# Kernel optimization log

Measured on AMD Instinct MI355X. Metric: run time of the kernel, lower is better.

The kernel has to match this reference:

```python
import jax, jax.numpy as jnp
import numpy as np

N_NODES = 50000
N_EDGES = 800000
D_IN = 128
D_OUT = 128
N_GRAPHS = 64
NEG_SLOPE = 0.01  # torch F.leaky_relu default


def gcn_conv(x, W, b, src, dst, n_nodes):
    """PyG GCNConv: linear, add self-loops, symmetric norm, scatter-add, bias."""
    h = x @ W  # [N, D_OUT]
    # degree including self-loop (edge_weight = 1)
    deg = jnp.zeros((n_nodes,), x.dtype).at[dst].add(1.0) + 1.0
    dinv = jax.lax.rsqrt(deg)
    norm = dinv[src] * dinv[dst]           # [E]
    agg = jnp.zeros_like(h).at[dst].add(h[src] * norm[:, None])
    # self-loop contribution: dinv[i]*dinv[i]*h[i] = h[i]/deg[i]
    return agg + h * (1.0 / deg)[:, None] + b


def gcn_branch(x, edge_index, Ws, bs):
    src, dst = edge_index[0], edge_index[1]
    n = x.shape[0]
    for W, b in zip(Ws, bs):
        x = gcn_conv(x, W, b, src, dst, n)
        x = jax.nn.leaky_relu(x, NEG_SLOPE)
        # dropout is identity in eval mode
    return x


def mean_pool(x, batch, num_graphs):
    s = jax.ops.segment_sum(x, batch, num_segments=num_graphs)
    cnt = jax.ops.segment_sum(jnp.ones((x.shape[0],), x.dtype), batch, num_segments=num_graphs)
    return s / jnp.maximum(cnt, 1.0)[:, None]


def setup_inputs() -> dict:
    key = jax.random.key(0)
    ks = jax.random.split(key, 20)
    inp = {
        'x1': jax.random.normal(ks[0], (N_NODES, D_IN), jnp.float32),
        'edge_index1': jax.random.randint(ks[1], (2, N_EDGES), 0, N_NODES, jnp.int64 if jax.config.jax_enable_x64 else jnp.int32),
        'batch1': jnp.sort(jax.random.randint(ks[2], (N_NODES,), 0, N_GRAPHS)),
        'x2': jax.random.normal(ks[3], (N_NODES, D_IN), jnp.float32),
        'edge_index2': jax.random.randint(ks[4], (2, N_EDGES), 0, N_NODES, jnp.int64 if jax.config.jax_enable_x64 else jnp.int32),
        'batch2': jnp.sort(jax.random.randint(ks[5], (N_NODES,), 0, N_GRAPHS)),
    }
    s = 1.0 / np.sqrt(D_IN)
    inp['W1_0'] = jax.random.uniform(ks[6], (D_IN, D_OUT), jnp.float32, -s, s)
    inp['b1_0'] = jnp.zeros((D_OUT,), jnp.float32)
    inp['W1_1'] = jax.random.uniform(ks[7], (D_OUT, D_OUT), jnp.float32, -s, s)
    inp['b1_1'] = jnp.zeros((D_OUT,), jnp.float32)
    inp['W2_0'] = jax.random.uniform(ks[8], (D_IN, D_OUT), jnp.float32, -s, s)
    inp['b2_0'] = jnp.zeros((D_OUT,), jnp.float32)
    inp['W2_1'] = jax.random.uniform(ks[9], (D_OUT, D_OUT), jnp.float32, -s, s)
    inp['b2_1'] = jnp.zeros((D_OUT,), jnp.float32)
    s2 = 1.0 / np.sqrt(2 * D_OUT)
    inp['lin1_W'] = jax.random.uniform(ks[10], (2 * D_OUT, D_OUT), jnp.float32, -s2, s2)
    inp['lin1_b'] = jax.random.uniform(ks[11], (D_OUT,), jnp.float32, -s2, s2)
    s3 = 1.0 / np.sqrt(D_OUT)
    inp['lin2_W'] = jax.random.uniform(ks[12], (D_OUT, 1), jnp.float32, -s3, s3)
    inp['lin2_b'] = jax.random.uniform(ks[13], (1,), jnp.float32, -s3, s3)
    return inp


def reference(x1, edge_index1, batch1, x2, edge_index2, batch2,
              W1_0, b1_0, W1_1, b1_1, W2_0, b2_0, W2_1, b2_1,
              lin1_W, lin1_b, lin2_W, lin2_b):
    h1 = gcn_branch(x1, edge_index1, [W1_0, W1_1], [b1_0, b1_1])
    h1 = mean_pool(h1, batch1, N_GRAPHS)
    h2 = gcn_branch(x2, edge_index2, [W2_0, W2_1], [b2_0, b2_1])
    h2 = mean_pool(h2, batch2, N_GRAPHS)
    h = jnp.concatenate([h1, h2], axis=-1)  # [G, 256]
    h = jax.nn.relu(h @ lin1_W + lin1_b)
    return h @ lin2_W + lin2_b  # [G, 1]
```

## Files before the change

### kernel.cpp

```cpp
#include <hip/hip_runtime.h>
#include <hip/hip_fp16.h>

#define N_NODES 50000
#define N_EDGES 800000
#define D 128
#define N_GRAPHS 64
#define NEG_SLOPE 0.01f
#define ELLW 32
#define OVF_CAP 8192

#define BUCKETS 196
#define NPAD (BUCKETS * 256)
#define EPB 4096
#define BCAP 5120
#define XS 136

typedef _Float16 half8 __attribute__((ext_vector_type(8)));
typedef _Float16 half4 __attribute__((ext_vector_type(4)));
typedef float f32x4 __attribute__((ext_vector_type(4)));
typedef float f32x2 __attribute__((ext_vector_type(2)));

__device__ __forceinline__ int lower_bound_i(const int* __restrict__ arr, int n, int key) {
    int lo = 0, hi = n;
    while (lo < hi) {
        int mid = (lo + hi) >> 1;
        if (arr[mid] < key) lo = mid + 1; else hi = mid;
    }
    return lo;
}

__global__ __launch_bounds__(256) void k_prep(const float* __restrict__ Wa, const float* __restrict__ Wb,
                                              const float* __restrict__ Wc, const float* __restrict__ Wd,
                                              const int* __restrict__ batch1, const int* __restrict__ batch2,
                                              __half* __restrict__ WtH, int* __restrict__ gcnt,
                                              float* __restrict__ pp, int* __restrict__ cntg) {
    const float* Ws[4] = {Wa, Wb, Wc, Wd};
    const float* W = Ws[blockIdx.x];
    __half* o = WtH + (size_t)blockIdx.x * 16384;
    int t = threadIdx.x;
    for (int r = 0; r < 64; r++) {
        int e = r * 256 + t;
        int k = e >> 7, n = e & 127;
        o[n * 128 + k] = __float2half(W[k * 128 + n]);
    }
#pragma unroll
    for (int i = 0; i < 16; i++) pp[blockIdx.x * 4096 + i * 256 + t] = 0.0f;
    if (blockIdx.x == 0) {
        for (int i = t; i < 2 * BUCKETS + 8; i += 256) gcnt[i] = 0;
    }
    if (blockIdx.x == 1) {
        if (t < 64)
            cntg[t] = lower_bound_i(batch1, N_NODES, t + 1) - lower_bound_i(batch1, N_NODES, t);
        else if (t < 128)
            cntg[t] = lower_bound_i(batch2, N_NODES, (t - 64) + 1) - lower_bound_i(batch2, N_NODES, t - 64);
    }
}

__global__ __launch_bounds__(256) void k_part(const int* __restrict__ ei1, const int* __restrict__ ei2,
                                              int* __restrict__ gcnt, int2* __restrict__ bucketed) {
    const int br = blockIdx.y;
    const int* __restrict__ src = (br ? ei2 : ei1);
    const int* __restrict__ dst = src + N_EDGES;
    int* __restrict__ gc = gcnt + br * BUCKETS;
    int2* __restrict__ bk = bucketed + (size_t)br * BUCKETS * BCAP;

    __shared__ int bcnt[BUCKETS];
    __shared__ int bofs[BUCKETS];
    __shared__ int gbase[BUCKETS];
    __shared__ int sc[BUCKETS];
    __shared__ int stot;
    __shared__ int2 stage[EPB];
    const int tid = threadIdx.x;
    const int base = blockIdx.x * EPB;
    for (int b = tid; b < BUCKETS; b += 256) bcnt[b] = 0;
    __syncthreads();
    int d_[16], s_[16], p_[16];
#pragma unroll
    for (int k = 0; k < 16; k++) {
        int i = base + k * 256 + tid;
        bool v = i < N_EDGES;
        d_[k] = v ? dst[i] : -1;
        s_[k] = v ? src[i] : 0;
        p_[k] = 0;
        if (v) p_[k] = atomicAdd(&bcnt[d_[k] >> 8], 1);
    }
    __syncthreads();
    if (tid < BUCKETS) sc[tid] = bcnt[tid];
    __syncthreads();
    for (int off = 1; off < BUCKETS; off <<= 1) {
        int v = (tid < BUCKETS && tid >= off) ? sc[tid - off] : 0;
        __syncthreads();
        if (tid < BUCKETS) sc[tid] += v;
        __syncthreads();
    }
    if (tid < BUCKETS) {
        bofs[tid] = sc[tid] - bcnt[tid];
        gbase[tid] = atomicAdd(&gc[tid], bcnt[tid]);
    }
    if (tid == BUCKETS - 1) stot = sc[tid];
    __syncthreads();
#pragma unroll
    for (int k = 0; k < 16; k++) {
        if (d_[k] >= 0) stage[bofs[d_[k] >> 8] + p_[k]] = make_int2(d_[k], s_[k]);
    }
    __syncthreads();
    int total = stot;
    for (int i = tid; i < total; i += 256) {
        int2 e = stage[i];
        int b = e.x >> 8;
        int dest = gbase[b] + (i - bofs[b]);
        if (dest < BCAP) bk[(size_t)b * BCAP + dest] = e;
    }
}

__global__ __launch_bounds__(256) void k_build(const int* __restrict__ gcnt, const int2* __restrict__ bucketed,
                                               int* __restrict__ cnti, unsigned short* __restrict__ ell,
                                               int2* __restrict__ ovf, int* __restrict__ ocnt) {
    const int br = blockIdx.y;
    const int* __restrict__ gc = gcnt + br * BUCKETS;
    const int2* __restrict__ bk = bucketed + (size_t)br * BUCKETS * BCAP;
    int* __restrict__ ci = cnti + br * NPAD;
    unsigned short* __restrict__ el = ell + (size_t)br * NPAD * ELLW;
    int2* __restrict__ ov = ovf + (size_t)br * OVF_CAP;
    int* __restrict__ oc = ocnt + br;

    __shared__ unsigned short lell[256 * ELLW];
    __shared__ int lcnt[256];
    const int b = blockIdx.x, tid = threadIdx.x;
    lcnt[tid] = 0;
    __syncthreads();
    int nb = min(gc[b], BCAP);
    const int2* __restrict__ bp = bk + (size_t)b * BCAP;
    for (int i = tid; i < nb; i += 256) {
        int2 e = bp[i];
        int dl = e.x & 255;
        int p = atomicAdd(&lcnt[dl], 1);
        if (p < ELLW) {
            lell[dl * ELLW + p] = (unsigned short)e.y;
        } else {
            int o = atomicAdd(oc, 1);
            if (o < OVF_CAP) ov[o] = e;
        }
    }
    __syncthreads();
    ci[b * 256 + tid] = lcnt[tid];
    uint4* eg = (uint4*)(el + (size_t)b * 256 * ELLW);
    const uint4* elc = (const uint4*)lell;
    for (int i = tid; i < 256 * ELLW * 2 / 16; i += 256) eg[i] = elc[i];
}

template <bool FP16IN>
__global__ __launch_bounds__(256) void k_gemm(const void* __restrict__ xin1, const void* __restrict__ xin2,
                                              const __half* __restrict__ WtHall, int layer,
                                              const int* __restrict__ cnti, unsigned char* __restrict__ H8) {
    const int br = blockIdx.y;
    const void* __restrict__ xin = (br ? xin2 : xin1);
    const __half* __restrict__ WtH = WtHall + (size_t)(br * 2 + layer) * 16384;
    const int* __restrict__ cnt = cnti + br * NPAD;
    unsigned char* __restrict__ h = H8 + (size_t)br * N_NODES * 128;

    __shared__ _Float16 Xl[64 * XS];
    __shared__ _Float16 Wt[128 * XS];
    const int tid = threadIdx.x;
    const int w = tid >> 6, lane = tid & 63;
    const int quad = lane >> 4, l16 = lane & 15;
    const int row0 = blockIdx.x * 64;

#pragma unroll
    for (int i = 0; i < 8; i++) {
        int i2 = tid + 256 * i;
        int r = i2 >> 4, cg = i2 & 15;
        *(uint4*)&Wt[r * XS + cg * 8] = ((const uint4*)WtH)[i2];
    }
    if (FP16IN) {
        const __half* x = (const __half*)xin;
#pragma unroll
        for (int i = 0; i < 4; i++) {
            int i2 = tid + 256 * i;
            int r = i2 >> 4, cg = i2 & 15;
            uint4 v = make_uint4(0, 0, 0, 0);
            if (row0 + r < N_NODES) v = ((const uint4*)(x + (size_t)(row0 + r) * D))[cg];
            *(uint4*)&Xl[r * XS + cg * 8] = v;
        }
    } else {
        const float* x = (const float*)xin;
#pragma unroll
        for (int i = 0; i < 8; i++) {
            int i2 = tid + 256 * i;
            int r = i2 >> 5, f4 = i2 & 31;
            float4 v = make_float4(0.f, 0.f, 0.f, 0.f);
            if (row0 + r < N_NODES) v = *(const float4*)((const float*)x + (size_t)(row0 + r) * D + f4 * 4);
            half4 hv;
            hv[0] = (_Float16)v.x; hv[1] = (_Float16)v.y; hv[2] = (_Float16)v.z; hv[3] = (_Float16)v.w;
            *(half4*)&Xl[r * XS + f4 * 4] = hv;
        }
    }
    __syncthreads();

    half8 a[4];
#pragma unroll
    for (int kb = 0; kb < 4; kb++)
        a[kb] = *(const half8*)&Xl[(w * 16 + l16) * XS + kb * 32 + quad * 8];

    const int rbase = row0 + w * 16 + quad * 4;
    float di[4];
#pragma unroll
    for (int reg = 0; reg < 4; reg++) {
        int r = rbase + reg;
        di[reg] = (r < N_NODES) ? rsqrtf((float)cnt[r] + 1.0f) : 0.0f;
    }

    float accs[8][4];
#pragma unroll
    for (int ct = 0; ct < 8; ct++) {
        f32x4 acc = {0.f, 0.f, 0.f, 0.f};
#pragma unroll
        for (int kb = 0; kb < 4; kb++) {
            half8 b = *(const half8*)&Wt[(ct * 16 + l16) * XS + kb * 32 + quad * 8];
            acc = __builtin_amdgcn_mfma_f32_16x16x32_f16(a[kb], b, acc, 0, 0, 0);
        }
#pragma unroll
        for (int reg = 0; reg < 4; reg++) accs[ct][reg] = acc[reg] * di[reg];
    }

    __syncthreads();
    unsigned char* S = (unsigned char*)Xl;
#pragma unroll
    for (int ct = 0; ct < 8; ct++)
#pragma unroll
        for (int reg = 0; reg < 4; reg++) {
            int p = __builtin_amdgcn_cvt_pk_fp8_f32(accs[ct][reg], accs[ct][reg], 0, false);
            S[(w * 16 + quad * 4 + reg) * 128 + ct * 16 + l16] = (unsigned char)p;
        }
    __syncthreads();
#pragma unroll
    for (int i = 0; i < 2; i++) {
        int idx = tid + 256 * i;
        int r = idx >> 3, cg = idx & 7;
        if (row0 + r < N_NODES)
            ((uint4*)(h + (size_t)(row0 + r) * 128))[cg] = ((const uint4*)S)[idx];
    }
}

__global__ __launch_bounds__(256) void k_agg(const int* __restrict__ cnti, const unsigned short* __restrict__ ell,
                                             const int2* __restrict__ ovf, const int* __restrict__ ocnt,
                                             const unsigned char* __restrict__ H8all, const float* __restrict__ bias1,
                                             const float* __restrict__ bias2, __half* __restrict__ ACT) {
    const int br = blockIdx.y;
    const int* __restrict__ cnt = cnti + br * NPAD;
    const unsigned short* __restrict__ el = ell + (size_t)br * NPAD * ELLW;
    const int2* __restrict__ ov = ovf + (size_t)br * OVF_CAP;
    const unsigned char* __restrict__ H8 = H8all + (size_t)br * N_NODES * 128;
    const float* __restrict__ bias = (br ? bias2 : bias1);
    __half* __restrict__ out = ACT + (size_t)br * N_NODES * D;

    const int tid = threadIdx.x;
    const int l32 = tid & 31;
    const int node = blockIdx.x * 8 + (tid >> 5);
    int n = cnt[node];
    int nc = min(n, ELLW);
    int sv = 0;
    if (l32 < nc) sv = (int)el[(size_t)node * ELLW + l32];
    int ncOther = __shfl(nc, (tid & 63) ^ 32, 64);
    int jmax = max(nc, ncOther);

    float4 acc[8];
    {
        unsigned int dw = *(const unsigned int*)(H8 + (size_t)node * 128 + l32 * 4);
        f32x2 lo = __builtin_amdgcn_cvt_pk_f32_fp8((int)dw, false);
        f32x2 hi = __builtin_amdgcn_cvt_pk_f32_fp8((int)dw, true);
        acc[0] = make_float4(lo[0], lo[1], hi[0], hi[1]);
    }
#pragma unroll
    for (int i = 1; i < 8; i++) acc[i] = make_float4(0.f, 0.f, 0.f, 0.f);

    for (int j = 0; j < jmax; j += 8) {
        int s[8]; float w[8];
#pragma unroll
        for (int i = 0; i < 8; i++) {
            s[i] = __shfl(sv, j + i, 32);
            w[i] = ((j + i) < nc) ? 1.0f : 0.0f;
        }
#pragma unroll
        for (int i = 0; i < 8; i++) {
            unsigned int dw = *(const unsigned int*)(H8 + (size_t)s[i] * 128 + l32 * 4);
            f32x2 lo = __builtin_amdgcn_cvt_pk_f32_fp8((int)dw, false);
            f32x2 hi = __builtin_amdgcn_cvt_pk_f32_fp8((int)dw, true);
            acc[i].x = fmaf(w[i], lo[0], acc[i].x);
            acc[i].y = fmaf(w[i], lo[1], acc[i].y);
            acc[i].z = fmaf(w[i], hi[0], acc[i].z);
            acc[i].w = fmaf(w[i], hi[1], acc[i].w);
        }
    }
    if (n > ELLW) {
        int oc = min(ocnt[br], OVF_CAP);
        for (int o = 0; o < oc; o++) {
            int2 p = ov[o];
            if (p.x == node) {
                unsigned int dw = *(const unsigned int*)(H8 + (size_t)p.y * 128 + l32 * 4);
                f32x2 lo = __builtin_amdgcn_cvt_pk_f32_fp8((int)dw, false);
                f32x2 hi = __builtin_amdgcn_cvt_pk_f32_fp8((int)dw, true);
                acc[0].x += lo[0]; acc[0].y += lo[1]; acc[0].z += hi[0]; acc[0].w += hi[1];
            }
        }
    }
    float sx = ((acc[0].x + acc[1].x) + (acc[2].x + acc[3].x)) + ((acc[4].x + acc[5].x) + (acc[6].x + acc[7].x));
    float sy = ((acc[0].y + acc[1].y) + (acc[2].y + acc[3].y)) + ((acc[4].y + acc[5].y) + (acc[6].y + acc[7].y));
    float sz = ((acc[0].z + acc[1].z) + (acc[2].z + acc[3].z)) + ((acc[4].z + acc[5].z) + (acc[6].z + acc[7].z));
    float sw = ((acc[0].w + acc[1].w) + (acc[2].w + acc[3].w)) + ((acc[4].w + acc[5].w) + (acc[6].w + acc[7].w));
    float dv = rsqrtf((float)n + 1.0f);
    float4 b = ((const float4*)bias)[l32];
    float vx = sx * dv + b.x;
    float vy = sy * dv + b.y;
    float vz = sz * dv + b.z;
    float vw = sw * dv + b.w;
    vx = vx > 0.0f ? vx : NEG_SLOPE * vx;
    vy = vy > 0.0f ? vy : NEG_SLOPE * vy;
    vz = vz > 0.0f ? vz : NEG_SLOPE * vz;
    vw = vw > 0.0f ? vw : NEG_SLOPE * vw;
    union { __half2 h2[2]; uint2 u; } up;
    up.h2[0] = __floats2half2_rn(vx, vy);
    up.h2[1] = __floats2half2_rn(vz, vw);
    *(uint2*)(out + (size_t)node * 128 + l32 * 4) = up.u;
}

__global__ __launch_bounds__(256) void k_aggpool(const int* __restrict__ cnti, const unsigned short* __restrict__ ell,
                                                 const int2* __restrict__ ovf, const int* __restrict__ ocnt,
                                                 const unsigned char* __restrict__ H8all,
                                                 const float* __restrict__ bias1, const float* __restrict__ bias2,
                                                 const int* __restrict__ batch1, const int* __restrict__ batch2,
                                                 float* __restrict__ ppall) {
    const int br = blockIdx.y;
    const int* __restrict__ cnt = cnti + br * NPAD;
    const unsigned short* __restrict__ el = ell + (size_t)br * NPAD * ELLW;
    const int2* __restrict__ ov = ovf + (size_t)br * OVF_CAP;
    const unsigned char* __restrict__ H8 = H8all + (size_t)br * N_NODES * 128;
    const float* __restrict__ bias = (br ? bias2 : bias1);
    const int* __restrict__ batch = (br ? batch2 : batch1);
    float* __restrict__ pp = ppall + (size_t)br * N_GRAPHS * D;

    const int tid = threadIdx.x;
    const int l32 = tid & 31;
    const int hw = tid >> 5;
    const int node = blockIdx.x * 8 + hw;
    int n = cnt[node];
    int nc = min(n, ELLW);
    int sv = 0;
    if (l32 < nc) sv = (int)el[(size_t)node * ELLW + l32];
    int ncOther = __shfl(nc, (tid & 63) ^ 32, 64);
    int jmax = max(nc, ncOther);

    float4 acc[8];
    {
        unsigned int dw = *(const unsigned int*)(H8 + (size_t)node * 128 + l32 * 4);
        f32x2 lo = __builtin_amdgcn_cvt_pk_f32_fp8((int)dw, false);
        f32x2 hi = __builtin_amdgcn_cvt_pk_f32_fp8((int)dw, true);
        acc[0] = make_float4(lo[0], lo[1], hi[0], hi[1]);
    }
#pragma unroll
    for (int i = 1; i < 8; i++) acc[i] = make_float4(0.f, 0.f, 0.f, 0.f);

    for (int j = 0; j < jmax; j += 8) {
        int s[8]; float wt[8];
#pragma unroll
        for (int i = 0; i < 8; i++) {
            s[i] = __shfl(sv, j + i, 32);
            wt[i] = ((j + i) < nc) ? 1.0f : 0.0f;
        }
#pragma unroll
        for (int i = 0; i < 8; i++) {
            unsigned int dw = *(const unsigned int*)(H8 + (size_t)s[i] * 128 + l32 * 4);
            f32x2 lo = __builtin_amdgcn_cvt_pk_f32_fp8((int)dw, false);
            f32x2 hi = __builtin_amdgcn_cvt_pk_f32_fp8((int)dw, true);
            acc[i].x = fmaf(wt[i], lo[0], acc[i].x);
            acc[i].y = fmaf(wt[i], lo[1], acc[i].y);
            acc[i].z = fmaf(wt[i], hi[0], acc[i].z);
            acc[i].w = fmaf(wt[i], hi[1], acc[i].w);
        }
    }
    if (n > ELLW) {
        int oc = min(ocnt[br], OVF_CAP);
        for (int o = 0; o < oc; o++) {
            int2 p = ov[o];
            if (p.x == node) {
                unsigned int dw = *(const unsigned int*)(H8 + (size_t)p.y * 128 + l32 * 4);
                f32x2 lo = __builtin_amdgcn_cvt_pk_f32_fp8((int)dw, false);
                f32x2 hi = __builtin_amdgcn_cvt_pk_f32_fp8((int)dw, true);
                acc[0].x += lo[0]; acc[0].y += lo[1]; acc[0].z += hi[0]; acc[0].w += hi[1];
            }
        }
    }
    float sx = ((acc[0].x + acc[1].x) + (acc[2].x + acc[3].x)) + ((acc[4].x + acc[5].x) + (acc[6].x + acc[7].x));
    float sy = ((acc[0].y + acc[1].y) + (acc[2].y + acc[3].y)) + ((acc[4].y + acc[5].y) + (acc[6].y + acc[7].y));
    float sz = ((acc[0].z + acc[1].z) + (acc[2].z + acc[3].z)) + ((acc[4].z + acc[5].z) + (acc[6].z + acc[7].z));
    float sw = ((acc[0].w + acc[1].w) + (acc[2].w + acc[3].w)) + ((acc[4].w + acc[5].w) + (acc[6].w + acc[7].w));
    float dv = rsqrtf((float)n + 1.0f);
    float4 b = ((const float4*)bias)[l32];
    float vx = sx * dv + b.x;
    float vy = sy * dv + b.y;
    float vz = sz * dv + b.z;
    float vw = sw * dv + b.w;
    vx = vx > 0.0f ? vx : NEG_SLOPE * vx;
    vy = vy > 0.0f ? vy : NEG_SLOPE * vy;
    vz = vz > 0.0f ? vz : NEG_SLOPE * vz;
    vw = vw > 0.0f ? vw : NEG_SLOPE * vw;
    __half2 q0 = __floats2half2_rn(vx, vy);
    __half2 q1 = __floats2half2_rn(vz, vw);
    float2 f0 = __half22float2(q0);
    float2 f1 = __half22float2(q1);

    __shared__ float sacc[8][128];
    __shared__ int sg[8];
    *(float4*)&sacc[hw][l32 * 4] = make_float4(f0.x, f0.y, f1.x, f1.y);
    if (l32 == 0) sg[hw] = batch[node];
    __syncthreads();
    if (tid < 128) {
        float s = sacc[0][tid];
        int g = sg[0];
        for (int r2 = 1; r2 < 8; r2++) {
            if (sg[r2] == g) {
                s += sacc[r2][tid];
            } else {
                atomicAdd(&pp[(size_t)g * D + tid], s);
                s = sacc[r2][tid];
                g = sg[r2];
            }
        }
        atomicAdd(&pp[(size_t)g * D + tid], s);
    }
}

__global__ __launch_bounds__(128) void k_mlp(const float* __restrict__ pp, const int* __restrict__ cntg,
                                             const float* __restrict__ lin1W, const float* __restrict__ lin1b,
                                             const float* __restrict__ lin2W, const float* __restrict__ lin2b,
                                             float* __restrict__ out) {
    int g = blockIdx.x;
    int c = threadIdx.x;
    __shared__ float cat[2 * D];
    cat[c] = pp[(size_t)g * D + c] / fmaxf((float)cntg[g], 1.0f);
    cat[c + D] = pp[(size_t)(N_GRAPHS + g) * D + c] / fmaxf((float)cntg[64 + g], 1.0f);
    __syncthreads();
    float acc = lin1b[c];
#pragma unroll 8
    for (int k = 0; k < 2 * D; k++) acc += cat[k] * lin1W[k * D + c];
    acc = fmaxf(acc, 0.0f);
    float v = acc * lin2W[c];
#pragma unroll
    for (int off = 32; off > 0; off >>= 1) v += __shfl_down(v, off, 64);
    __shared__ float wsum[2];
    if ((c & 63) == 0) wsum[c >> 6] = v;
    __syncthreads();
    if (c == 0) out[g] = wsum[0] + wsum[1] + lin2b[0];
}

extern "C" void kernel_launch(void* const* d_in, const int* in_sizes, int n_in,
                              void* d_out, int out_size, void* d_ws, size_t ws_size,
                              hipStream_t stream) {
    const float* x1 = (const float*)d_in[0];
    const int*   ei1 = (const int*)d_in[1];
    const int*   batch1 = (const int*)d_in[2];
    const float* x2 = (const float*)d_in[3];
    const int*   ei2 = (const int*)d_in[4];
    const int*   batch2 = (const int*)d_in[5];
    const float* W1_0 = (const float*)d_in[6];
    const float* b1_0 = (const float*)d_in[7];
    const float* W1_1 = (const float*)d_in[8];
    const float* b1_1 = (const float*)d_in[9];
    const float* W2_0 = (const float*)d_in[10];
    const float* b2_0 = (const float*)d_in[11];
    const float* W2_1 = (const float*)d_in[12];
    const float* b2_1 = (const float*)d_in[13];
    const float* lin1W = (const float*)d_in[14];
    const float* lin1b = (const float*)d_in[15];
    const float* lin2W = (const float*)d_in[16];
    const float* lin2b = (const float*)d_in[17];
    float* out = (float*)d_out;

    __half* WtH = (__half*)d_ws;
    __half* ACT = WtH + 65536;
    unsigned char* H8a = (unsigned char*)(ACT + 2 * (size_t)N_NODES * D);
    unsigned char* H8b = H8a + 2 * (size_t)N_NODES * 128;
    unsigned short* ell = (unsigned short*)(H8b + 2 * (size_t)N_NODES * 128);
    int2*   bucketed = (int2*)(ell + 2 * (size_t)NPAD * ELLW);
    int*    cnti = (int*)(bucketed + 2 * (size_t)BUCKETS * BCAP);
    int*    gcnt = cnti + 2 * NPAD;
    int*    ocnt = gcnt + 2 * BUCKETS;
    int*    cntg = ocnt + 8;
    int2*   ovf  = (int2*)(cntg + 128);
    float*  pp   = (float*)(ovf + 2 * (size_t)OVF_CAP);

    dim3 b256(256);
    int partBlocks = (N_EDGES + EPB - 1) / EPB;
    int gemmBlocks = (N_NODES + 63) / 64;
    int aggBlocks  = N_NODES / 8;

    k_prep<<<4, b256, 0, stream>>>(W1_0, W1_1, W2_0, W2_1, batch1, batch2, WtH, gcnt, pp, cntg);

    k_part  <<<dim3(partBlocks, 2), b256, 0, stream>>>(ei1, ei2, gcnt, bucketed);
    k_build <<<dim3(BUCKETS, 2),    b256, 0, stream>>>(gcnt, bucketed, cnti, ell, ovf, ocnt);

    k_gemm<false><<<dim3(gemmBlocks, 2), b256, 0, stream>>>(x1, x2, WtH, 0, cnti, H8a);
    k_agg        <<<dim3(aggBlocks, 2),  b256, 0, stream>>>(cnti, ell, ovf, ocnt, H8a, b1_0, b2_0, ACT);
    k_gemm<true> <<<dim3(gemmBlocks, 2), b256, 0, stream>>>(ACT, ACT + (size_t)N_NODES * D, WtH, 1, cnti, H8b);
    k_aggpool    <<<dim3(aggBlocks, 2),  b256, 0, stream>>>(cnti, ell, ovf, ocnt, H8b, b1_1, b2_1, batch1, batch2, pp);

    k_mlp<<<N_GRAPHS, dim3(128), 0, stream>>>(pp, cntg, lin1W, lin1b, lin2W, lin2b, out);
}
```

Baseline: 288.6 us.

## Double-buffer neighbor gathers in aggregation, interleave branches, shrink partition blocks

The aggregation kernels now stage each block's neighbor index lists in shared memory and gather neighbor rows with a two-buffer software pipeline over groups of 8. The next group's loads are issued before the current group is accumulated, which is meant to hide gather latency. Branch selection moves from the grid y dimension to interleaving on blockIdx.x. The edge partition kernel processes half as many edges per block to gain more parallelism. The ELL build also zero-fills its shared staging, so unused slots hold index 0 rather than stale data; zero-weight padding slots then read row 0 instead of arbitrary rows. The fixed unroll up to 32 neighbors adds register pressure and code size.

After: 281.2 us, median of 2. 1.03x faster.

```diff
diff --git a/kernel.cpp b/kernel.cpp
--- a/kernel.cpp
+++ b/kernel.cpp
@@ -11,7 +11,7 @@
 
 #define BUCKETS 196
 #define NPAD (BUCKETS * 256)
-#define EPB 4096
+#define EPB 2048
 #define BCAP 5120
 #define XS 136
 
@@ -58,7 +58,8 @@
 
 __global__ __launch_bounds__(256) void k_part(const int* __restrict__ ei1, const int* __restrict__ ei2,
                                               int* __restrict__ gcnt, int2* __restrict__ bucketed) {
-    const int br = blockIdx.y;
+    const int br = blockIdx.x & 1;
+    const int blk = blockIdx.x >> 1;
     const int* __restrict__ src = (br ? ei2 : ei1);
     const int* __restrict__ dst = src + N_EDGES;
     int* __restrict__ gc = gcnt + br * BUCKETS;
@@ -71,12 +72,12 @@
     __shared__ int stot;
     __shared__ int2 stage[EPB];
     const int tid = threadIdx.x;
-    const int base = blockIdx.x * EPB;
+    const int base = blk * EPB;
     for (int b = tid; b < BUCKETS; b += 256) bcnt[b] = 0;
     __syncthreads();
-    int d_[16], s_[16], p_[16];
-#pragma unroll
-    for (int k = 0; k < 16; k++) {
+    int d_[8], s_[8], p_[8];
+#pragma unroll
+    for (int k = 0; k < 8; k++) {
         int i = base + k * 256 + tid;
         bool v = i < N_EDGES;
         d_[k] = v ? dst[i] : -1;
@@ -100,7 +101,7 @@
     if (tid == BUCKETS - 1) stot = sc[tid];
     __syncthreads();
 #pragma unroll
-    for (int k = 0; k < 16; k++) {
+    for (int k = 0; k < 8; k++) {
         if (d_[k] >= 0) stage[bofs[d_[k] >> 8] + p_[k]] = make_int2(d_[k], s_[k]);
     }
     __syncthreads();
@@ -116,7 +117,8 @@
 __global__ __launch_bounds__(256) void k_build(const int* __restrict__ gcnt, const int2* __restrict__ bucketed,
                                                int* __restrict__ cnti, unsigned short* __restrict__ ell,
                                                int2* __restrict__ ovf, int* __restrict__ ocnt) {
-    const int br = blockIdx.y;
+    const int br = blockIdx.x & 1;
+    const int b = blockIdx.x >> 1;
     const int* __restrict__ gc = gcnt + br * BUCKETS;
     const int2* __restrict__ bk = bucketed + (size_t)br * BUCKETS * BCAP;
     int* __restrict__ ci = cnti + br * NPAD;
@@ -126,8 +128,10 @@
 
     __shared__ unsigned short lell[256 * ELLW];
     __shared__ int lcnt[256];
-    const int b = blockIdx.x, tid = threadIdx.x;
+    const int tid = threadIdx.x;
     lcnt[tid] = 0;
+#pragma unroll
+    for (int i = 0; i < 4; i++) ((uint4*)lell)[tid + 256 * i] = make_uint4(0u, 0u, 0u, 0u);
     __syncthreads();
     int nb = min(gc[b], BCAP);
     const int2* __restrict__ bp = bk + (size_t)b * BCAP;
@@ -242,11 +246,67 @@
     }
 }
 
+#define AGG_ISSUE(buf, g) do {                                                             \
+    unsigned int iw0 = *(const unsigned int*)&sidx[hw][(g) * 8 + 0];                       \
+    unsigned int iw1 = *(const unsigned int*)&sidx[hw][(g) * 8 + 2];                       \
+    unsigned int iw2 = *(const unsigned int*)&sidx[hw][(g) * 8 + 4];                       \
+    unsigned int iw3 = *(const unsigned int*)&sidx[hw][(g) * 8 + 6];                       \
+    buf[0] = *(const unsigned int*)(H8 + (size_t)(iw0 & 0xffffu) * 128 + l32 * 4);         \
+    buf[1] = *(const unsigned int*)(H8 + (size_t)(iw0 >> 16) * 128 + l32 * 4);             \
+    buf[2] = *(const unsigned int*)(H8 + (size_t)(iw1 & 0xffffu) * 128 + l32 * 4);         \
+    buf[3] = *(const unsigned int*)(H8 + (size_t)(iw1 >> 16) * 128 + l32 * 4);             \
+    buf[4] = *(const unsigned int*)(H8 + (size_t)(iw2 & 0xffffu) * 128 + l32 * 4);         \
+    buf[5] = *(const unsigned int*)(H8 + (size_t)(iw2 >> 16) * 128 + l32 * 4);             \
+    buf[6] = *(const unsigned int*)(H8 + (size_t)(iw3 & 0xffffu) * 128 + l32 * 4);         \
+    buf[7] = *(const unsigned int*)(H8 + (size_t)(iw3 >> 16) * 128 + l32 * 4);             \
+} while (0)
+
+#define AGG_CONSUME(buf, g) do {                                                           \
+    _Pragma("unroll")                                                                      \
+    for (int i_ = 0; i_ < 8; i_++) {                                                       \
+        float wt = ((g) * 8 + i_ < nc) ? 1.0f : 0.0f;                                      \
+        f32x2 lo = __builtin_amdgcn_cvt_pk_f32_fp8((int)buf[i_], false);                   \
+        f32x2 hi = __builtin_amdgcn_cvt_pk_f32_fp8((int)buf[i_], true);                    \
+        accv[i_ & 3].x = fmaf(wt, lo[0], accv[i_ & 3].x);                                  \
+        accv[i_ & 3].y = fmaf(wt, lo[1], accv[i_ & 3].y);                                  \
+        accv[i_ & 3].z = fmaf(wt, hi[0], accv[i_ & 3].z);                                  \
+        accv[i_ & 3].w = fmaf(wt, hi[1], accv[i_ & 3].w);                                  \
+    }                                                                                      \
+} while (0)
+
+#define AGG_CORE()                                                                         \
+    float4 accv[4];                                                                        \
+    {                                                                                      \
+        f32x2 lo = __builtin_amdgcn_cvt_pk_f32_fp8((int)dself, false);                     \
+        f32x2 hi = __builtin_amdgcn_cvt_pk_f32_fp8((int)dself, true);                      \
+        accv[0] = make_float4(lo[0], lo[1], hi[0], hi[1]);                                 \
+    }                                                                                      \
+    accv[1] = make_float4(0.f, 0.f, 0.f, 0.f); accv[2] = accv[1]; accv[3] = accv[1];       \
+    unsigned int b0_[8], b1_[8];                                                           \
+    AGG_ISSUE(b0_, 0);                                                                     \
+    if (jmax > 8) { AGG_ISSUE(b1_, 1); }                                                   \
+    AGG_CONSUME(b0_, 0);                                                                   \
+    if (jmax > 8) {                                                                        \
+        if (jmax > 16) { AGG_ISSUE(b0_, 2); }                                              \
+        AGG_CONSUME(b1_, 1);                                                               \
+        if (jmax > 16) {                                                                   \
+            if (jmax > 24) { AGG_ISSUE(b1_, 3); }                                          \
+            AGG_CONSUME(b0_, 2);                                                           \
+            if (jmax > 24) { AGG_CONSUME(b1_, 3); }                                        \
+        }                                                                                  \
+    }
+
 __global__ __launch_bounds__(256) void k_agg(const int* __restrict__ cnti, const unsigned short* __restrict__ ell,
                                              const int2* __restrict__ ovf, const int* __restrict__ ocnt,
                                              const unsigned char* __restrict__ H8all, const float* __restrict__ bias1,
                                              const float* __restrict__ bias2, __half* __restrict__ ACT) {
-    const int br = blockIdx.y;
+    const int tid = threadIdx.x;
+    const int l32 = tid & 31;
+    const int hw = tid >> 5;
+    const int br = blockIdx.x & 1;
+    const int blk = blockIdx.x >> 1;
+    const int node = blk * 8 + hw;
+
     const int* __restrict__ cnt = cnti + br * NPAD;
     const unsigned short* __restrict__ el = ell + (size_t)br * NPAD * ELLW;
     const int2* __restrict__ ov = ovf + (size_t)br * OVF_CAP;
@@ -254,44 +314,18 @@
     const float* __restrict__ bias = (br ? bias2 : bias1);
     __half* __restrict__ out = ACT + (size_t)br * N_NODES * D;
 
-    const int tid = threadIdx.x;
-    const int l32 = tid & 31;
-    const int node = blockIdx.x * 8 + (tid >> 5);
+    __shared__ unsigned short sidx[8][ELLW];
+    if (tid < 32) ((uint4*)sidx)[tid] = ((const uint4*)(el + (size_t)blk * 8 * ELLW))[tid];
+
     int n = cnt[node];
     int nc = min(n, ELLW);
-    int sv = 0;
-    if (l32 < nc) sv = (int)el[(size_t)node * ELLW + l32];
-    int ncOther = __shfl(nc, (tid & 63) ^ 32, 64);
-    int jmax = max(nc, ncOther);
-
-    float4 acc[8];
-    {
-        unsigned int dw = *(const unsigned int*)(H8 + (size_t)node * 128 + l32 * 4);
-        f32x2 lo = __builtin_amdgcn_cvt_pk_f32_fp8((int)dw, false);
-        f32x2 hi = __builtin_amdgcn_cvt_pk_f32_fp8((int)dw, true);
-        acc[0] = make_float4(lo[0], lo[1], hi[0], hi[1]);
-    }
-#pragma unroll
-    for (int i = 1; i < 8; i++) acc[i] = make_float4(0.f, 0.f, 0.f, 0.f);
-
-    for (int j = 0; j < jmax; j += 8) {
-        int s[8]; float w[8];
-#pragma unroll
-        for (int i = 0; i < 8; i++) {
-            s[i] = __shfl(sv, j + i, 32);
-            w[i] = ((j + i) < nc) ? 1.0f : 0.0f;
-        }
-#pragma unroll
-        for (int i = 0; i < 8; i++) {
-            unsigned int dw = *(const unsigned int*)(H8 + (size_t)s[i] * 128 + l32 * 4);
-            f32x2 lo = __builtin_amdgcn_cvt_pk_f32_fp8((int)dw, false);
-            f32x2 hi = __builtin_amdgcn_cvt_pk_f32_fp8((int)dw, true);
-            acc[i].x = fmaf(w[i], lo[0], acc[i].x);
-            acc[i].y = fmaf(w[i], lo[1], acc[i].y);
-            acc[i].z = fmaf(w[i], hi[0], acc[i].z);
-            acc[i].w = fmaf(w[i], hi[1], acc[i].w);
-        }
-    }
+    int ncO = __shfl(nc, (tid & 63) ^ 32, 64);
+    int jmax = max(nc, ncO);
+    unsigned int dself = *(const unsigned int*)(H8 + (size_t)node * 128 + l32 * 4);
+    __syncthreads();
+
+    AGG_CORE();
+
     if (n > ELLW) {
         int oc = min(ocnt[br], OVF_CAP);
         for (int o = 0; o < oc; o++) {
@@ -300,14 +334,14 @@
                 unsigned int dw = *(const unsigned int*)(H8 + (size_t)p.y * 128 + l32 * 4);
                 f32x2 lo = __builtin_amdgcn_cvt_pk_f32_fp8((int)dw, false);
                 f32x2 hi = __builtin_amdgcn_cvt_pk_f32_fp8((int)dw, true);
-                acc[0].x += lo[0]; acc[0].y += lo[1]; acc[0].z += hi[0]; acc[0].w += hi[1];
+                accv[0].x += lo[0]; accv[0].y += lo[1]; accv[0].z += hi[0]; accv[0].w += hi[1];
             }
         }
     }
-    float sx = ((acc[0].x + acc[1].x) + (acc[2].x + acc[3].x)) + ((acc[4].x + acc[5].x) + (acc[6].x + acc[7].x));
-    float sy = ((acc[0].y + acc[1].y) + (acc[2].y + acc[3].y)) + ((acc[4].y + acc[5].y) + (acc[6].y + acc[7].y));
-    float sz = ((acc[0].z + acc[1].z) + (acc[2].z + acc[3].z)) + ((acc[4].z + acc[5].z) + (acc[6].z + acc[7].z));
-    float sw = ((acc[0].w + acc[1].w) + (acc[2].w + acc[3].w)) + ((acc[4].w + acc[5].w) + (acc[6].w + acc[7].w));
+    float sx = (accv[0].x + accv[1].x) + (accv[2].x + accv[3].x);
+    float sy = (accv[0].y + accv[1].y) + (accv[2].y + accv[3].y);
+    float sz = (accv[0].z + accv[1].z) + (accv[2].z + accv[3].z);
+    float sw = (accv[0].w + accv[1].w) + (accv[2].w + accv[3].w);
     float dv = rsqrtf((float)n + 1.0f);
     float4 b = ((const float4*)bias)[l32];
     float vx = sx * dv + b.x;
@@ -330,7 +364,13 @@
                                                  const float* __restrict__ bias1, const float* __restrict__ bias2,
                                                  const int* __restrict__ batch1, const int* __restrict__ batch2,
                                                  float* __restrict__ ppall) {
-    const int br = blockIdx.y;
+    const int tid = threadIdx.x;
+    const int l32 = tid & 31;
+    const int hw = tid >> 5;
+    const int br = blockIdx.x & 1;
+    const int blk = blockIdx.x >> 1;
+    const int node = blk * 8 + hw;
+
     const int* __restrict__ cnt = cnti + br * NPAD;
     const unsigned short* __restrict__ el = ell + (size_t)br * NPAD * ELLW;
     const int2* __restrict__ ov = ovf + (size_t)br * OVF_CAP;
@@ -339,45 +379,18 @@
     const int* __restrict__ batch = (br ? batch2 : batch1);
     float* __restrict__ pp = ppall + (size_t)br * N_GRAPHS * D;
 
-    const int tid = threadIdx.x;
-    const int l32 = tid & 31;
-    const int hw = tid >> 5;
-    const int node = blockIdx.x * 8 + hw;
+    __shared__ unsigned short sidx[8][ELLW];
+    if (tid < 32) ((uint4*)sidx)[tid] = ((const uint4*)(el + (size_t)blk * 8 * ELLW))[tid];
+
     int n = cnt[node];
     int nc = min(n, ELLW);
-    int sv = 0;
-    if (l32 < nc) sv = (int)el[(size_t)node * ELLW + l32];
-    int ncOther = __shfl(nc, (tid & 63) ^ 32, 64);
-    int jmax = max(nc, ncOther);
-
-    float4 acc[8];
-    {
-        unsigned int dw = *(const unsigned int*)(H8 + (size_t)node * 128 + l32 * 4);
-        f32x2 lo = __builtin_amdgcn_cvt_pk_f32_fp8((int)dw, false);
-        f32x2 hi = __builtin_amdgcn_cvt_pk_f32_fp8((int)dw, true);
-        acc[0] = make_float4(lo[0], lo[1], hi[0], hi[1]);
-    }
-#pragma unroll
-    for (int i = 1; i < 8; i++) acc[i] = make_float4(0.f, 0.f, 0.f, 0.f);
-
-    for (int j = 0; j < jmax; j += 8) {
-        int s[8]; float wt[8];
-#pragma unroll
-        for (int i = 0; i < 8; i++) {
-            s[i] = __shfl(sv, j + i, 32);
-            wt[i] = ((j + i) < nc) ? 1.0f : 0.0f;
-        }
-#pragma unroll
-        for (int i = 0; i < 8; i++) {
-            unsigned int dw = *(const unsigned int*)(H8 + (size_t)s[i] * 128 + l32 * 4);
-            f32x2 lo = __builtin_amdgcn_cvt_pk_f32_fp8((int)dw, false);
-            f32x2 hi = __builtin_amdgcn_cvt_pk_f32_fp8((int)dw, true);
-            acc[i].x = fmaf(wt[i], lo[0], acc[i].x);
-            acc[i].y = fmaf(wt[i], lo[1], acc[i].y);
-            acc[i].z = fmaf(wt[i], hi[0], acc[i].z);
-            acc[i].w = fmaf(wt[i], hi[1], acc[i].w);
-        }
-    }
+    int ncO = __shfl(nc, (tid & 63) ^ 32, 64);
+    int jmax = max(nc, ncO);
+    unsigned int dself = *(const unsigned int*)(H8 + (size_t)node * 128 + l32 * 4);
+    __syncthreads();
+
+    AGG_CORE();
+
     if (n > ELLW) {
         int oc = min(ocnt[br], OVF_CAP);
         for (int o = 0; o < oc; o++) {
@@ -386,14 +399,14 @@
                 unsigned int dw = *(const unsigned int*)(H8 + (size_t)p.y * 128 + l32 * 4);
                 f32x2 lo = __builtin_amdgcn_cvt_pk_f32_fp8((int)dw, false);
                 f32x2 hi = __builtin_amdgcn_cvt_pk_f32_fp8((int)dw, true);
-                acc[0].x += lo[0]; acc[0].y += lo[1]; acc[0].z += hi[0]; acc[0].w += hi[1];
+                accv[0].x += lo[0]; accv[0].y += lo[1]; accv[0].z += hi[0]; accv[0].w += hi[1];
             }
         }
     }
-    float sx = ((acc[0].x + acc[1].x) + (acc[2].x + acc[3].x)) + ((acc[4].x + acc[5].x) + (acc[6].x + acc[7].x));
-    float sy = ((acc[0].y + acc[1].y) + (acc[2].y + acc[3].y)) + ((acc[4].y + acc[5].y) + (acc[6].y + acc[7].y));
-    float sz = ((acc[0].z + acc[1].z) + (acc[2].z + acc[3].z)) + ((acc[4].z + acc[5].z) + (acc[6].z + acc[7].z));
-    float sw = ((acc[0].w + acc[1].w) + (acc[2].w + acc[3].w)) + ((acc[4].w + acc[5].w) + (acc[6].w + acc[7].w));
+    float sx = (accv[0].x + accv[1].x) + (accv[2].x + accv[3].x);
+    float sy = (accv[0].y + accv[1].y) + (accv[2].y + accv[3].y);
+    float sz = (accv[0].z + accv[1].z) + (accv[2].z + accv[3].z);
+    float sw = (accv[0].w + accv[1].w) + (accv[2].w + accv[3].w);
     float dv = rsqrtf((float)n + 1.0f);
     float4 b = ((const float4*)bias)[l32];
     float vx = sx * dv + b.x;
@@ -496,13 +509,13 @@
 
     k_prep<<<4, b256, 0, stream>>>(W1_0, W1_1, W2_0, W2_1, batch1, batch2, WtH, gcnt, pp, cntg);
 
-    k_part  <<<dim3(partBlocks, 2), b256, 0, stream>>>(ei1, ei2, gcnt, bucketed);
-    k_build <<<dim3(BUCKETS, 2),    b256, 0, stream>>>(gcnt, bucketed, cnti, ell, ovf, ocnt);
+    k_part  <<<partBlocks * 2, b256, 0, stream>>>(ei1, ei2, gcnt, bucketed);
+    k_build <<<BUCKETS * 2,    b256, 0, stream>>>(gcnt, bucketed, cnti, ell, ovf, ocnt);
 
     k_gemm<false><<<dim3(gemmBlocks, 2), b256, 0, stream>>>(x1, x2, WtH, 0, cnti, H8a);
-    k_agg        <<<dim3(aggBlocks, 2),  b256, 0, stream>>>(cnti, ell, ovf, ocnt, H8a, b1_0, b2_0, ACT);
+    k_agg        <<<aggBlocks * 2,       b256, 0, stream>>>(cnti, ell, ovf, ocnt, H8a, b1_0, b2_0, ACT);
     k_gemm<true> <<<dim3(gemmBlocks, 2), b256, 0, stream>>>(ACT, ACT + (size_t)N_NODES * D, WtH, 1, cnti, H8b);
-    k_aggpool    <<<dim3(aggBlocks, 2),  b256, 0, stream>>>(cnti, ell, ovf, ocnt, H8b, b1_1, b2_1, batch1, batch2, pp);
+    k_aggpool    <<<aggBlocks * 2,       b256, 0, stream>>>(cnti, ell, ovf, ocnt, H8b, b1_1, b2_1, batch1, batch2, pp);
 
     k_mlp<<<N_GRAPHS, dim3(128), 0, stream>>>(pp, cntg, lin1W, lin1b, lin2W, lin2b, out);
 }
```
